# Kernel tuning notes

Measured on AMD Instinct MI355X. Metric: run time of the kernel, lower is better.

## Reference

```python
import jax, jax.numpy as jnp
import numpy as np
from jax import lax

B, T, LM, H = 16, 60, 63, 64   # batch, frames, landmark dim, lstm hidden
IMG_H, IMG_W = 240, 320
CONV_FEAT = 252                 # 4 * 7 * 9


def _conv(x, w, b, s):
    # x: [N, Cin, H, W], w: [Cout, Cin, kh, kw], VALID padding, stride s
    y = lax.conv_general_dilated(x, w, (s, s), 'VALID',
                                 dimension_numbers=('NCHW', 'OIHW', 'NCHW'))
    return y + b[None, :, None, None]


def setup_inputs() -> dict:
    key = jax.random.key(0)
    ks = jax.random.split(key, 24)
    s = 0.05
    d = {
        'input': jax.random.normal(ks[0], (B, T, LM), jnp.float32),
        'video': jax.random.uniform(ks[1], (B, T, IMG_H, IMG_W), jnp.float32),
        'W00': jax.random.normal(ks[2], (LM, LM), jnp.float32) * s,
        'b00': jnp.zeros((LM,), jnp.float32),
        'W01': jax.random.normal(ks[3], (64, LM), jnp.float32) * s,
        'b01': jnp.zeros((64,), jnp.float32),
        'Wc0': jax.random.normal(ks[4], (16, 1, 5, 5), jnp.float32) * s,
        'bc0': jnp.zeros((16,), jnp.float32),
        'Wc1': jax.random.normal(ks[5], (16, 16, 5, 5), jnp.float32) * s,
        'bc1': jnp.zeros((16,), jnp.float32),
        'Wc2': jax.random.normal(ks[6], (4, 16, 2, 2), jnp.float32) * s,
        'bc2': jnp.zeros((4,), jnp.float32),
        'Wih': jax.random.normal(ks[7], (4 * H, 64 + CONV_FEAT), jnp.float32) * s,
        'Whh': jax.random.normal(ks[8], (4 * H, H), jnp.float32) * s,
        'bih': jnp.zeros((4 * H,), jnp.float32),
        'bhh': jnp.zeros((4 * H,), jnp.float32),
        'W10': jax.random.normal(ks[9], (32, H), jnp.float32) * s,
        'b10': jnp.zeros((32,), jnp.float32),
        'W11': jax.random.normal(ks[10], (32, 32), jnp.float32) * s,
        'b11': jnp.zeros((32,), jnp.float32),
        'W12': jax.random.normal(ks[11], (256, 32), jnp.float32) * s,
        'b12': jnp.zeros((256,), jnp.float32),
    }
    return d


def reference(input, video, W00, b00, W01, b01, Wc0, bc0, Wc1, bc1, Wc2, bc2,
              Wih, Whh, bih, bhh, W10, b10, W11, b11, W12, b12):
    relu = jax.nn.relu
    # per-frame landmark MLP, vectorized over all frames: [B, T, 64]
    f = relu(jnp.einsum('btl,ml->btm', input, W00) + b00)
    f = relu(jnp.einsum('btl,ml->btm', f, W01) + b01)
    # per-frame conv features, all frames in one batched conv: [B*T, 1, 240, 320]
    v = video.reshape(B * T, 1, IMG_H, IMG_W)
    v = relu(_conv(v, Wc0, bc0, 4))          # [B*T, 16, 59, 79]
    v = relu(_conv(v, Wc1, bc1, 4))          # [B*T, 16, 14, 19]
    v = relu(_conv(v, Wc2, bc2, 2))          # [B*T, 4, 7, 9]
    v = v.reshape(B, T, CONV_FEAT)
    # frame inputs to LSTM: [B, T, 316]
    x = jnp.concatenate([f, v], axis=-1)
    # Torch semantics: LSTM called unbatched with 2D input [B, 316] per frame,
    # so the batch dim is consumed as a sequence; state carries across frames.
    # Total sequence is frame-major: [T, B, 316] -> [T*B, 316].
    seq = x.transpose(1, 0, 2).reshape(T * B, -1)

    def step(carry, xt):
        h, c = carry
        g = xt @ Wih.T + bih + h @ Whh.T + bhh
        i, fg, gg, o = jnp.split(g, 4)
        c = jax.nn.sigmoid(fg) * c + jax.nn.sigmoid(i) * jnp.tanh(gg)
        h = jax.nn.sigmoid(o) * jnp.tanh(c)
        return (h, c), h

    h0 = jnp.zeros((H,), seq.dtype)
    _, hs = lax.scan(step, (h0, h0), seq)    # [T*B, H]
    out = hs[-B:]                            # last frame's full output: [B, H]
    out = relu(out @ W10.T + b10)
    out = relu(out @ W11.T + b11)
    return out @ W12.T + b12                 # [B, 256]
```

## Files before the change

kernel.cpp:

```cpp
#include <hip/hip_runtime.h>
#include <math.h>

#define B_   16
#define T_   60
#define LMD  63
#define IH   240
#define IW   320
#define XDIM 316
#define NSEQ 960

#define X_BYTES   1213440
#define G_BYTES   983040

__device__ __forceinline__ float rl(float v, int k) {
    return __uint_as_float((unsigned)__builtin_amdgcn_readlane((int)__float_as_uint(v), k));
}
__device__ __forceinline__ float sig_f(float x) {
    return __builtin_amdgcn_rcpf(1.0f + __expf(-x));
}
__device__ __forceinline__ float tanh_f(float x) {
    return 1.0f - 2.0f * __builtin_amdgcn_rcpf(__expf(2.0f * x) + 1.0f);
}

__global__ void k_mlp(const float* __restrict__ inp,
                      const float* __restrict__ W00, const float* __restrict__ b00,
                      const float* __restrict__ W01, const float* __restrict__ b01,
                      float* __restrict__ X) {
    __shared__ float x0s[LMD], f1s[LMD];
    int bt = blockIdx.x;
    int b = bt / T_, t = bt % T_;
    int s = t * B_ + b;
    int m = threadIdx.x;
    if (m < LMD) x0s[m] = inp[bt * LMD + m];
    __syncthreads();
    if (m < LMD) {
        const float* wr = W00 + m * LMD;
        float a0 = 0.f, a1 = 0.f, a2 = 0.f, a3 = 0.f;
        for (int k = 0; k < 60; k += 4) {
            a0 += x0s[k + 0] * wr[k + 0];
            a1 += x0s[k + 1] * wr[k + 1];
            a2 += x0s[k + 2] * wr[k + 2];
            a3 += x0s[k + 3] * wr[k + 3];
        }
        a0 += x0s[60] * wr[60]; a1 += x0s[61] * wr[61]; a2 += x0s[62] * wr[62];
        f1s[m] = fmaxf(((a0 + a1) + (a2 + a3)) + b00[m], 0.f);
    }
    __syncthreads();
    {
        const float* wr = W01 + m * LMD;
        float a0 = 0.f, a1 = 0.f, a2 = 0.f, a3 = 0.f;
        for (int k = 0; k < 60; k += 4) {
            a0 += f1s[k + 0] * wr[k + 0];
            a1 += f1s[k + 1] * wr[k + 1];
            a2 += f1s[k + 2] * wr[k + 2];
            a3 += f1s[k + 3] * wr[k + 3];
        }
        a0 += f1s[60] * wr[60]; a1 += f1s[61] * wr[61]; a2 += f1s[62] * wr[62];
        X[(size_t)s * XDIM + m] = fmaxf(((a0 + a1) + (a2 + a3)) + b01[m], 0.f);
    }
}

__global__ __launch_bounds__(256, 1) void k_conv(const float* __restrict__ video,
        const float* __restrict__ Wc0, const float* __restrict__ bc0,
        const float* __restrict__ Wc1, const float* __restrict__ bc1,
        const float* __restrict__ Wc2, const float* __restrict__ bc2,
        float* __restrict__ X) {
    __shared__ float W0T[26 * 16];
    __shared__ float band[16 * 408];
    __shared__ float part[19 * 4 * 17];
    __shared__ float c1L[14 * 19 * 17];
    int tid = threadIdx.x;
    int bt = blockIdx.x;
    int b = bt / T_, t = bt % T_;
    int s = t * B_ + b;
    const float* vid = video + (size_t)bt * (IH * IW);

    int ch1 = tid & 15, ic = tid >> 4;
    int wave = tid >> 6, lane = tid & 63;

    int d0 = tid / 79, c0c0 = tid % 79;
    int pos1 = tid + 256;
    bool has1 = (pos1 < 395);
    int d1 = has1 ? pos1 / 79 : 0, c0c1 = has1 ? pos1 % 79 : 0;

    for (int i = tid; i < 400; i += 256) { int ch = i / 25, tap = i % 25; W0T[tap * 16 + ch] = Wc0[i]; }
    if (tid < 16) W0T[25 * 16 + tid] = bc0[tid];
    float w1r[25];
#pragma unroll
    for (int tap = 0; tap < 25; ++tap)
        w1r[tap] = Wc1[(ch1 * 16 + ic) * 25 + tap];

    float PX0[25], PX1[25];
    {
        const float* vb = vid + (4 * d0) * IW + c0c0 * 4;
#pragma unroll
        for (int kr = 0; kr < 5; ++kr) {
            float4 v = *(const float4*)(vb + kr * IW);
            PX0[kr*5+0]=v.x; PX0[kr*5+1]=v.y; PX0[kr*5+2]=v.z; PX0[kr*5+3]=v.w;
            PX0[kr*5+4]=vb[kr*IW+4];
        }
        if (has1) {
            const float* vc = vid + (4 * d1) * IW + c0c1 * 4;
#pragma unroll
            for (int kr = 0; kr < 5; ++kr) {
                float4 v = *(const float4*)(vc + kr * IW);
                PX1[kr*5+0]=v.x; PX1[kr*5+1]=v.y; PX1[kr*5+2]=v.z; PX1[kr*5+3]=v.w;
                PX1[kr*5+4]=vc[kr*IW+4];
            }
        }
    }
    __syncthreads();

    for (int r1 = 0; r1 < 14; ++r1) {
        {
            float acc[16];
            {
                const float4* b4 = (const float4*)&W0T[25 * 16];
                float4 ba = b4[0], bb = b4[1], bc = b4[2], bd = b4[3];
                acc[0]=ba.x; acc[1]=ba.y; acc[2]=ba.z; acc[3]=ba.w;
                acc[4]=bb.x; acc[5]=bb.y; acc[6]=bb.z; acc[7]=bb.w;
                acc[8]=bc.x; acc[9]=bc.y; acc[10]=bc.z; acc[11]=bc.w;
                acc[12]=bd.x; acc[13]=bd.y; acc[14]=bd.z; acc[15]=bd.w;
            }
#pragma unroll
            for (int tap = 0; tap < 25; ++tap) {
                float p = PX0[tap];
                const float4* w4 = (const float4*)&W0T[tap * 16];
                float4 wa = w4[0], wb = w4[1], wc = w4[2], wd = w4[3];
                acc[0]+=p*wa.x; acc[1]+=p*wa.y; acc[2]+=p*wa.z; acc[3]+=p*wa.w;
                acc[4]+=p*wb.x; acc[5]+=p*wb.y; acc[6]+=p*wb.z; acc[7]+=p*wb.w;
                acc[8]+=p*wc.x; acc[9]+=p*wc.y; acc[10]+=p*wc.z; acc[11]+=p*wc.w;
                acc[12]+=p*wd.x; acc[13]+=p*wd.y; acc[14]+=p*wd.z; acc[15]+=p*wd.w;
            }
#pragma unroll
            for (int ch = 0; ch < 16; ++ch)
                band[ch * 408 + d0 * 80 + c0c0] = fmaxf(acc[ch], 0.f);
        }
        if (has1) {
            float acc[16];
            {
                const float4* b4 = (const float4*)&W0T[25 * 16];
                float4 ba = b4[0], bb = b4[1], bc = b4[2], bd = b4[3];
                acc[0]=ba.x; acc[1]=ba.y; acc[2]=ba.z; acc[3]=ba.w;
                acc[4]=bb.x; acc[5]=bb.y; acc[6]=bb.z; acc[7]=bb.w;
                acc[8]=bc.x; acc[9]=bc.y; acc[10]=bc.z; acc[11]=bc.w;
                acc[12]=bd.x; acc[13]=bd.y; acc[14]=bd.z; acc[15]=bd.w;
            }
#pragma unroll
            for (int tap = 0; tap < 25; ++tap) {
                float p = PX1[tap];
                const float4* w4 = (const float4*)&W0T[tap * 16];
                float4 wa = w4[0], wb = w4[1], wc = w4[2], wd = w4[3];
                acc[0]+=p*wa.x; acc[1]+=p*wa.y; acc[2]+=p*wa.z; acc[3]+=p*wa.w;
                acc[4]+=p*wb.x; acc[5]+=p*wb.y; acc[6]+=p*wb.z; acc[7]+=p*wb.w;
                acc[8]+=p*wc.x; acc[9]+=p*wc.y; acc[10]+=p*wc.z; acc[11]+=p*wc.w;
                acc[12]+=p*wd.x; acc[13]+=p*wd.y; acc[14]+=p*wd.z; acc[15]+=p*wd.w;
            }
#pragma unroll
            for (int ch = 0; ch < 16; ++ch)
                band[ch * 408 + d1 * 80 + c0c1] = fmaxf(acc[ch], 0.f);
        }

        if (r1 + 1 < 14) {
            const float* vb = vid + (16 * (r1+1) + 4 * d0) * IW + c0c0 * 4;
#pragma unroll
            for (int kr = 0; kr < 5; ++kr) {
                float4 v = *(const float4*)(vb + kr * IW);
                PX0[kr*5+0]=v.x; PX0[kr*5+1]=v.y; PX0[kr*5+2]=v.z; PX0[kr*5+3]=v.w;
                PX0[kr*5+4]=vb[kr*IW+4];
            }
            if (has1) {
                const float* vc = vid + (16 * (r1+1) + 4 * d1) * IW + c0c1 * 4;
#pragma unroll
                for (int kr = 0; kr < 5; ++kr) {
                    float4 v = *(const float4*)(vc + kr * IW);
                    PX1[kr*5+0]=v.x; PX1[kr*5+1]=v.y; PX1[kr*5+2]=v.z; PX1[kr*5+3]=v.w;
                    PX1[kr*5+4]=vc[kr*IW+4];
                }
            }
        }
        __syncthreads();

        const float* bb0 = &band[ic * 408];
        for (int c1c = 0; c1c < 19; ++c1c) {
            const float* bb = bb0 + c1c * 4;
            float a0, a1, a2, a3, a4;
            {
                float4 v = *(const float4*)(bb);       float sc = bb[4];
                a0 = v.x*w1r[0]  + v.y*w1r[1]  + v.z*w1r[2]  + v.w*w1r[3]  + sc*w1r[4];
            }
            {
                float4 v = *(const float4*)(bb + 80);  float sc = bb[84];
                a1 = v.x*w1r[5]  + v.y*w1r[6]  + v.z*w1r[7]  + v.w*w1r[8]  + sc*w1r[9];
            }
            {
                float4 v = *(const float4*)(bb + 160); float sc = bb[164];
                a2 = v.x*w1r[10] + v.y*w1r[11] + v.z*w1r[12] + v.w*w1r[13] + sc*w1r[14];
            }
            {
                float4 v = *(const float4*)(bb + 240); float sc = bb[244];
                a3 = v.x*w1r[15] + v.y*w1r[16] + v.z*w1r[17] + v.w*w1r[18] + sc*w1r[19];
            }
            {
                float4 v = *(const float4*)(bb + 320); float sc = bb[324];
                a4 = v.x*w1r[20] + v.y*w1r[21] + v.z*w1r[22] + v.w*w1r[23] + sc*w1r[24];
            }
            float p = ((a0 + a1) + (a2 + a3)) + a4;
            p += __shfl_xor(p, 16);
            p += __shfl_xor(p, 32);
            if (lane < 16)
                part[c1c * 68 + wave * 17 + ch1] = p;
        }
        __syncthreads();

        for (int o = tid; o < 304; o += 256) {
            int c1c = o >> 4, ch = o & 15;
            const float* pp = &part[c1c * 68 + ch];
            float v = bc1[ch] + pp[0] + pp[17] + pp[34] + pp[51];
            c1L[(r1 * 19 + c1c) * 17 + ch] = fmaxf(v, 0.f);
        }
        __syncthreads();
    }

    for (int o = tid; o < 252; o += 256) {
        int ch2 = o / 63, rr = (o / 9) % 7, cc = o % 9;
        float a = bc2[ch2];
        for (int ic2 = 0; ic2 < 16; ++ic2)
            for (int kr = 0; kr < 2; ++kr)
                for (int kc = 0; kc < 2; ++kc)
                    a += c1L[((2 * rr + kr) * 19 + 2 * cc + kc) * 17 + ic2] *
                         Wc2[((ch2 * 16 + ic2) * 2 + kr) * 2 + kc];
        X[(size_t)s * XDIM + 64 + o] = fmaxf(a, 0.f);
    }
}

__global__ void k_gpre(const float* __restrict__ X, const float* __restrict__ Wih,
                       const float* __restrict__ bih, const float* __restrict__ bhh,
                       float* __restrict__ G) {
    int s = blockIdx.x;
    int j = threadIdx.x;
    const float4* x4 = (const float4*)(X + (size_t)s * XDIM);
    const float4* w4 = (const float4*)(Wih + (size_t)j * XDIM);
    float a0 = 0.f, a1 = 0.f, a2 = 0.f, a3 = 0.f;
    for (int ko = 0; ko < 79; ++ko) {
        float4 w = w4[ko], x = x4[ko];
        a0 += w.x * x.x;
        a1 += w.y * x.y;
        a2 += w.z * x.z;
        a3 += w.w * x.w;
    }
    G[(size_t)s * 256 + j] = ((a0 + a1) + (a2 + a3)) + (bih[j] + bhh[j]);
}

#define REPW(M) M(0) M(1) M(2) M(3) M(4) M(5) M(6) M(7) \
                M(8) M(9) M(10) M(11) M(12) M(13) M(14) M(15)

__global__ __launch_bounds__(256)
__attribute__((amdgpu_waves_per_eu(1, 1)))
void k_scan(const float* __restrict__ G,
        const float* __restrict__ Whh,
        const float* __restrict__ W10, const float* __restrict__ b10,
        const float* __restrict__ W11, const float* __restrict__ b11,
        const float* __restrict__ W12, const float* __restrict__ b12,
        float* __restrict__ out) {
    __shared__ float act[2][256];
    __shared__ float hsL[16 * 64];
    __shared__ float m1s[32], m2s[32];
    int j = threadIdx.x;
    int w = j >> 6, l = j & 63;

#define DECLW(n) float4 wv##n;
    REPW(DECLW)
#undef DECLW
    {
        const float4* Wr = (const float4*)(Whh + (size_t)j * 64);
#define LOADW(n) wv##n = Wr[n];
        REPW(LOADW)
#undef LOADW
    }

    float h = 0.f, c = 0.f;
    float gcur = G[j];

#define STEPBODY(GNEXT_EXPR)                                              \
    {                                                                     \
        float gnext = (GNEXT_EXPR);                                       \
        float a0 = gcur, a1 = 0.f, a2 = 0.f, a3 = 0.f;                    \
        REPW(GFMA)                                                        \
        float g = (a0 + a1) + (a2 + a3);                                  \
        float av = (w == 2) ? tanh_f(g) : sig_f(g);                       \
        act[t & 1][j] = av;                                               \
        asm volatile("s_waitcnt lgkmcnt(0)\n\ts_barrier" ::: "memory");   \
        const float* ab = act[t & 1];                                     \
        float ai = ab[l], af = ab[64 + l], ag = ab[128 + l], ao = ab[192 + l]; \
        c = af * c + ai * ag;                                             \
        h = ao * tanh_f(c);                                               \
        gcur = gnext;                                                     \
    }
#define GFMA(n) {                                                         \
        float h0 = rl(h, 4*(n)+0), h1 = rl(h, 4*(n)+1);                   \
        float h2 = rl(h, 4*(n)+2), h3 = rl(h, 4*(n)+3);                   \
        a0 += h0 * wv##n.x; a1 += h1 * wv##n.y;                           \
        a2 += h2 * wv##n.z; a3 += h3 * wv##n.w;                           \
    }

    for (int t = 0; t < NSEQ - 16; ++t) {
        STEPBODY(G[(size_t)(t + 1) * 256 + j])
    }
    for (int t = NSEQ - 16; t < NSEQ; ++t) {
        STEPBODY((t + 1 < NSEQ) ? G[(size_t)(t + 1) * 256 + j] : 0.f)
        if (w == 0) hsL[(t - (NSEQ - 16)) * 64 + l] = h;
    }
#undef GFMA
#undef STEPBODY
    __syncthreads();

    for (int r = 0; r < 16; ++r) {
        if (j < 32) {
            float a = b10[j];
            for (int k = 0; k < 64; ++k) a += hsL[r * 64 + k] * W10[j * 64 + k];
            m1s[j] = fmaxf(a, 0.f);
        }
        __syncthreads();
        if (j < 32) {
            float a = b11[j];
            for (int k = 0; k < 32; ++k) a += m1s[k] * W11[j * 32 + k];
            m2s[j] = fmaxf(a, 0.f);
        }
        __syncthreads();
        {
            float a = b12[j];
            for (int k = 0; k < 32; ++k) a += m2s[k] * W12[j * 32 + k];
            out[r * 256 + j] = a;
        }
        __syncthreads();
    }
}

extern "C" void kernel_launch(void* const* d_in, const int* in_sizes, int n_in,
                              void* d_out, int out_size, void* d_ws, size_t ws_size,
                              hipStream_t stream) {
    const float* inp   = (const float*)d_in[0];
    const float* video = (const float*)d_in[1];
    const float* W00   = (const float*)d_in[2];
    const float* b00   = (const float*)d_in[3];
    const float* W01   = (const float*)d_in[4];
    const float* b01   = (const float*)d_in[5];
    const float* Wc0   = (const float*)d_in[6];
    const float* bc0   = (const float*)d_in[7];
    const float* Wc1   = (const float*)d_in[8];
    const float* bc1   = (const float*)d_in[9];
    const float* Wc2   = (const float*)d_in[10];
    const float* bc2   = (const float*)d_in[11];
    const float* Wih   = (const float*)d_in[12];
    const float* Whh   = (const float*)d_in[13];
    const float* bih   = (const float*)d_in[14];
    const float* bhh   = (const float*)d_in[15];
    const float* W10   = (const float*)d_in[16];
    const float* b10   = (const float*)d_in[17];
    const float* W11   = (const float*)d_in[18];
    const float* b11   = (const float*)d_in[19];
    const float* W12   = (const float*)d_in[20];
    const float* b12   = (const float*)d_in[21];

    float* X = (float*)d_ws;
    float* G = (float*)((char*)d_ws + X_BYTES);

    k_mlp <<<NSEQ, 64, 0, stream>>>(inp, W00, b00, W01, b01, X);
    k_conv<<<NSEQ, 256, 0, stream>>>(video, Wc0, bc0, Wc1, bc1, Wc2, bc2, X);
    k_gpre<<<NSEQ, 256, 0, stream>>>(X, Wih, bih, bhh, G);
    k_scan<<<1, 256, 0, stream>>>(G, Whh, W10, b10, W11, b11, W12, b12, (float*)d_out);
}
```

Baseline: 715.8 us.

## Fuse landmark MLP, conv stack and input-gate projection into one kernel

Merges the per-frame MLP, the conv feature extractor and the Wih input projection into a single kernel per sequence position, keeping the 316-wide feature row in shared memory instead of writing X to global memory and reading it back. This drops two kernel launches and the X round trip. Launch bounds are raised from 1 to 3 blocks per CU, which may constrain registers for the conv stage. Block indexing is changed to be frame-major.

```diff
diff --git a/kernel.cpp b/kernel.cpp
--- a/kernel.cpp
+++ b/kernel.cpp
@@ -9,7 +9,6 @@
 #define XDIM 316
 #define NSEQ 960
 
-#define X_BYTES   1213440
 #define G_BYTES   983040
 
 __device__ __forceinline__ float rl(float v, int k) {
@@ -22,19 +21,46 @@
     return 1.0f - 2.0f * __builtin_amdgcn_rcpf(__expf(2.0f * x) + 1.0f);
 }
 
-__global__ void k_mlp(const float* __restrict__ inp,
-                      const float* __restrict__ W00, const float* __restrict__ b00,
-                      const float* __restrict__ W01, const float* __restrict__ b01,
-                      float* __restrict__ X) {
-    __shared__ float x0s[LMD], f1s[LMD];
-    int bt = blockIdx.x;
-    int b = bt / T_, t = bt % T_;
-    int s = t * B_ + b;
-    int m = threadIdx.x;
-    if (m < LMD) x0s[m] = inp[bt * LMD + m];
-    __syncthreads();
-    if (m < LMD) {
-        const float* wr = W00 + m * LMD;
+__global__ __launch_bounds__(256, 3) void k_prod(
+        const float* __restrict__ inp,  const float* __restrict__ video,
+        const float* __restrict__ W00,  const float* __restrict__ b00,
+        const float* __restrict__ W01,  const float* __restrict__ b01,
+        const float* __restrict__ Wc0,  const float* __restrict__ bc0,
+        const float* __restrict__ Wc1,  const float* __restrict__ bc1,
+        const float* __restrict__ Wc2,  const float* __restrict__ bc2,
+        const float* __restrict__ Wih,  const float* __restrict__ bih,
+        const float* __restrict__ bhh,  float* __restrict__ G)
+{
+    __shared__ float W0T[26 * 16];
+    __shared__ float band[16 * 408];
+    __shared__ float part[19 * 4 * 17];
+    __shared__ float c1L[14 * 19 * 17];
+    __shared__ __align__(16) float xrow[XDIM];
+    __shared__ float x0s[64], f1s[64];
+    int tid = threadIdx.x;
+    int s = blockIdx.x;
+    int t = s >> 4, b = s & 15;
+    int bt = b * T_ + t;
+    const float* vid = video + (size_t)bt * (IH * IW);
+
+    int ch1 = tid & 15, ic = tid >> 4;
+    int wave = tid >> 6, lane = tid & 63;
+    int d0 = tid / 79, c0c0 = tid % 79;
+    int pos1 = tid + 256;
+    bool has1 = (pos1 < 395);
+    int d1 = has1 ? pos1 / 79 : 0, c0c1 = has1 ? pos1 % 79 : 0;
+
+    for (int i = tid; i < 400; i += 256) { int ch = i / 25, tap = i % 25; W0T[tap * 16 + ch] = Wc0[i]; }
+    if (tid < 16) W0T[25 * 16 + tid] = bc0[tid];
+    float w1r[25];
+#pragma unroll
+    for (int tap = 0; tap < 25; ++tap)
+        w1r[tap] = Wc1[(ch1 * 16 + ic) * 25 + tap];
+
+    if (tid < LMD) x0s[tid] = inp[bt * LMD + tid];
+    __syncthreads();
+    if (tid < LMD) {
+        const float* wr = W00 + tid * LMD;
         float a0 = 0.f, a1 = 0.f, a2 = 0.f, a3 = 0.f;
         for (int k = 0; k < 60; k += 4) {
             a0 += x0s[k + 0] * wr[k + 0];
@@ -43,11 +69,11 @@
             a3 += x0s[k + 3] * wr[k + 3];
         }
         a0 += x0s[60] * wr[60]; a1 += x0s[61] * wr[61]; a2 += x0s[62] * wr[62];
-        f1s[m] = fmaxf(((a0 + a1) + (a2 + a3)) + b00[m], 0.f);
-    }
-    __syncthreads();
-    {
-        const float* wr = W01 + m * LMD;
+        f1s[tid] = fmaxf(((a0 + a1) + (a2 + a3)) + b00[tid], 0.f);
+    }
+    __syncthreads();
+    if (tid < 64) {
+        const float* wr = W01 + tid * LMD;
         float a0 = 0.f, a1 = 0.f, a2 = 0.f, a3 = 0.f;
         for (int k = 0; k < 60; k += 4) {
             a0 += f1s[k + 0] * wr[k + 0];
@@ -56,39 +82,8 @@
             a3 += f1s[k + 3] * wr[k + 3];
         }
         a0 += f1s[60] * wr[60]; a1 += f1s[61] * wr[61]; a2 += f1s[62] * wr[62];
-        X[(size_t)s * XDIM + m] = fmaxf(((a0 + a1) + (a2 + a3)) + b01[m], 0.f);
-    }
-}
-
-__global__ __launch_bounds__(256, 1) void k_conv(const float* __restrict__ video,
-        const float* __restrict__ Wc0, const float* __restrict__ bc0,
-        const float* __restrict__ Wc1, const float* __restrict__ bc1,
-        const float* __restrict__ Wc2, const float* __restrict__ bc2,
-        float* __restrict__ X) {
-    __shared__ float W0T[26 * 16];
-    __shared__ float band[16 * 408];
-    __shared__ float part[19 * 4 * 17];
-    __shared__ float c1L[14 * 19 * 17];
-    int tid = threadIdx.x;
-    int bt = blockIdx.x;
-    int b = bt / T_, t = bt % T_;
-    int s = t * B_ + b;
-    const float* vid = video + (size_t)bt * (IH * IW);
-
-    int ch1 = tid & 15, ic = tid >> 4;
-    int wave = tid >> 6, lane = tid & 63;
-
-    int d0 = tid / 79, c0c0 = tid % 79;
-    int pos1 = tid + 256;
-    bool has1 = (pos1 < 395);
-    int d1 = has1 ? pos1 / 79 : 0, c0c1 = has1 ? pos1 % 79 : 0;
-
-    for (int i = tid; i < 400; i += 256) { int ch = i / 25, tap = i % 25; W0T[tap * 16 + ch] = Wc0[i]; }
-    if (tid < 16) W0T[25 * 16 + tid] = bc0[tid];
-    float w1r[25];
-#pragma unroll
-    for (int tap = 0; tap < 25; ++tap)
-        w1r[tap] = Wc1[(ch1 * 16 + ic) * 25 + tap];
+        xrow[tid] = fmaxf(((a0 + a1) + (a2 + a3)) + b01[tid], 0.f);
+    }
 
     float PX0[25], PX1[25];
     {
@@ -230,26 +225,23 @@
                 for (int kc = 0; kc < 2; ++kc)
                     a += c1L[((2 * rr + kr) * 19 + 2 * cc + kc) * 17 + ic2] *
                          Wc2[((ch2 * 16 + ic2) * 2 + kr) * 2 + kc];
-        X[(size_t)s * XDIM + 64 + o] = fmaxf(a, 0.f);
-    }
-}
-
-__global__ void k_gpre(const float* __restrict__ X, const float* __restrict__ Wih,
-                       const float* __restrict__ bih, const float* __restrict__ bhh,
-                       float* __restrict__ G) {
-    int s = blockIdx.x;
-    int j = threadIdx.x;
-    const float4* x4 = (const float4*)(X + (size_t)s * XDIM);
-    const float4* w4 = (const float4*)(Wih + (size_t)j * XDIM);
-    float a0 = 0.f, a1 = 0.f, a2 = 0.f, a3 = 0.f;
-    for (int ko = 0; ko < 79; ++ko) {
-        float4 w = w4[ko], x = x4[ko];
-        a0 += w.x * x.x;
-        a1 += w.y * x.y;
-        a2 += w.z * x.z;
-        a3 += w.w * x.w;
-    }
-    G[(size_t)s * 256 + j] = ((a0 + a1) + (a2 + a3)) + (bih[j] + bhh[j]);
+        xrow[64 + o] = fmaxf(a, 0.f);
+    }
+    __syncthreads();
+
+    {
+        const float4* x4 = (const float4*)xrow;
+        const float4* w4 = (const float4*)(Wih + (size_t)tid * XDIM);
+        float a0 = 0.f, a1 = 0.f, a2 = 0.f, a3 = 0.f;
+        for (int ko = 0; ko < 79; ++ko) {
+            float4 w = w4[ko], x = x4[ko];
+            a0 += w.x * x.x;
+            a1 += w.y * x.y;
+            a2 += w.z * x.z;
+            a3 += w.w * x.w;
+        }
+        G[(size_t)s * 256 + tid] = ((a0 + a1) + (a2 + a3)) + (bih[tid] + bhh[tid]);
+    }
 }
 
 #define REPW(M) M(0) M(1) M(2) M(3) M(4) M(5) M(6) M(7) \
@@ -363,11 +355,10 @@
     const float* W12   = (const float*)d_in[20];
     const float* b12   = (const float*)d_in[21];
 
-    float* X = (float*)d_ws;
-    float* G = (float*)((char*)d_ws + X_BYTES);
-
-    k_mlp <<<NSEQ, 64, 0, stream>>>(inp, W00, b00, W01, b01, X);
-    k_conv<<<NSEQ, 256, 0, stream>>>(video, Wc0, bc0, Wc1, bc1, Wc2, bc2, X);
-    k_gpre<<<NSEQ, 256, 0, stream>>>(X, Wih, bih, bhh, G);
+    float* G = (float*)d_ws;
+
+    k_prod<<<NSEQ, 256, 0, stream>>>(inp, video, W00, b00, W01, b01,
+                                     Wc0, bc0, Wc1, bc1, Wc2, bc2,
+                                     Wih, bih, bhh, G);
     k_scan<<<1, 256, 0, stream>>>(G, Whh, W10, b10, W11, b11, W12, b12, (float*)d_out);
 }
```

Measured after the change: 724.6 us. No clear change (+1.2%).

## Keep conv0 weights in registers and split output channels across thread quads

Applied to the files above, without the earlier changes.

The first conv stage drops the shared-memory transposed weight table. Each thread now holds 4 output channels' 25-tap weights in registers, and groups of 4 threads split the 16 channels for one output position, looping over 7 positions per band. Launch bounds are raised to allow 3 blocks per CU. The register prefetch of the next band's pixels is removed, so global loads now sit directly in the compute loop, and each pixel is loaded by 4 threads instead of 1. The aim is to cut LDS weight reads and raise occupancy, at the cost of more global load traffic and possible register spills under the tighter bound.

```diff
diff --git a/kernel.cpp b/kernel.cpp
--- a/kernel.cpp
+++ b/kernel.cpp
@@ -60,12 +60,11 @@
     }
 }
 
-__global__ __launch_bounds__(256, 1) void k_conv(const float* __restrict__ video,
+__global__ __launch_bounds__(256, 3) void k_conv(const float* __restrict__ video,
         const float* __restrict__ Wc0, const float* __restrict__ bc0,
         const float* __restrict__ Wc1, const float* __restrict__ bc1,
         const float* __restrict__ Wc2, const float* __restrict__ bc2,
         float* __restrict__ X) {
-    __shared__ float W0T[26 * 16];
     __shared__ float band[16 * 408];
     __shared__ float part[19 * 4 * 17];
     __shared__ float c1L[14 * 19 * 17];
@@ -78,105 +77,57 @@
     int ch1 = tid & 15, ic = tid >> 4;
     int wave = tid >> 6, lane = tid & 63;
 
-    int d0 = tid / 79, c0c0 = tid % 79;
-    int pos1 = tid + 256;
-    bool has1 = (pos1 < 395);
-    int d1 = has1 ? pos1 / 79 : 0, c0c1 = has1 ? pos1 % 79 : 0;
-
-    for (int i = tid; i < 400; i += 256) { int ch = i / 25, tap = i % 25; W0T[tap * 16 + ch] = Wc0[i]; }
-    if (tid < 16) W0T[25 * 16 + tid] = bc0[tid];
+    int q = tid & 3, pgrp = tid >> 2;
+
+    float w0a[25], w0b[25], w0c[25], w0d[25];
+#pragma unroll
+    for (int tap = 0; tap < 25; ++tap) {
+        w0a[tap] = Wc0[(4 * q + 0) * 25 + tap];
+        w0b[tap] = Wc0[(4 * q + 1) * 25 + tap];
+        w0c[tap] = Wc0[(4 * q + 2) * 25 + tap];
+        w0d[tap] = Wc0[(4 * q + 3) * 25 + tap];
+    }
+    float b0a = bc0[4 * q + 0], b0b = bc0[4 * q + 1];
+    float b0c = bc0[4 * q + 2], b0d = bc0[4 * q + 3];
+
     float w1r[25];
 #pragma unroll
     for (int tap = 0; tap < 25; ++tap)
         w1r[tap] = Wc1[(ch1 * 16 + ic) * 25 + tap];
 
-    float PX0[25], PX1[25];
-    {
-        const float* vb = vid + (4 * d0) * IW + c0c0 * 4;
-#pragma unroll
-        for (int kr = 0; kr < 5; ++kr) {
-            float4 v = *(const float4*)(vb + kr * IW);
-            PX0[kr*5+0]=v.x; PX0[kr*5+1]=v.y; PX0[kr*5+2]=v.z; PX0[kr*5+3]=v.w;
-            PX0[kr*5+4]=vb[kr*IW+4];
-        }
-        if (has1) {
-            const float* vc = vid + (4 * d1) * IW + c0c1 * 4;
-#pragma unroll
-            for (int kr = 0; kr < 5; ++kr) {
-                float4 v = *(const float4*)(vc + kr * IW);
-                PX1[kr*5+0]=v.x; PX1[kr*5+1]=v.y; PX1[kr*5+2]=v.z; PX1[kr*5+3]=v.w;
-                PX1[kr*5+4]=vc[kr*IW+4];
-            }
-        }
-    }
-    __syncthreads();
-
     for (int r1 = 0; r1 < 14; ++r1) {
         {
-            float acc[16];
-            {
-                const float4* b4 = (const float4*)&W0T[25 * 16];
-                float4 ba = b4[0], bb = b4[1], bc = b4[2], bd = b4[3];
-                acc[0]=ba.x; acc[1]=ba.y; acc[2]=ba.z; acc[3]=ba.w;
-                acc[4]=bb.x; acc[5]=bb.y; acc[6]=bb.z; acc[7]=bb.w;
-                acc[8]=bc.x; acc[9]=bc.y; acc[10]=bc.z; acc[11]=bc.w;
-                acc[12]=bd.x; acc[13]=bd.y; acc[14]=bd.z; acc[15]=bd.w;
-            }
+            int d = 0, c0c = pgrp;
 #pragma unroll
-            for (int tap = 0; tap < 25; ++tap) {
-                float p = PX0[tap];
-                const float4* w4 = (const float4*)&W0T[tap * 16];
-                float4 wa = w4[0], wb = w4[1], wc = w4[2], wd = w4[3];
-                acc[0]+=p*wa.x; acc[1]+=p*wa.y; acc[2]+=p*wa.z; acc[3]+=p*wa.w;
-                acc[4]+=p*wb.x; acc[5]+=p*wb.y; acc[6]+=p*wb.z; acc[7]+=p*wb.w;
-                acc[8]+=p*wc.x; acc[9]+=p*wc.y; acc[10]+=p*wc.z; acc[11]+=p*wc.w;
-                acc[12]+=p*wd.x; acc[13]+=p*wd.y; acc[14]+=p*wd.z; acc[15]+=p*wd.w;
-            }
+            for (int i = 0; i < 7; ++i) {
+                if (i < 6 || pgrp < 11) {
+                    const float* vb = vid + (16 * r1 + 4 * d) * IW + c0c * 4;
+                    float aa = b0a, ab = b0b, ac = b0c, ad = b0d;
 #pragma unroll
-            for (int ch = 0; ch < 16; ++ch)
-                band[ch * 408 + d0 * 80 + c0c0] = fmaxf(acc[ch], 0.f);
-        }
-        if (has1) {
-            float acc[16];
-            {
-                const float4* b4 = (const float4*)&W0T[25 * 16];
-                float4 ba = b4[0], bb = b4[1], bc = b4[2], bd = b4[3];
-                acc[0]=ba.x; acc[1]=ba.y; acc[2]=ba.z; acc[3]=ba.w;
-                acc[4]=bb.x; acc[5]=bb.y; acc[6]=bb.z; acc[7]=bb.w;
-                acc[8]=bc.x; acc[9]=bc.y; acc[10]=bc.z; acc[11]=bc.w;
-                acc[12]=bd.x; acc[13]=bd.y; acc[14]=bd.z; acc[15]=bd.w;
-            }
-#pragma unroll
-            for (int tap = 0; tap < 25; ++tap) {
-                float p = PX1[tap];
-                const float4* w4 = (const float4*)&W0T[tap * 16];
-                float4 wa = w4[0], wb = w4[1], wc = w4[2], wd = w4[3];
-                acc[0]+=p*wa.x; acc[1]+=p*wa.y; acc[2]+=p*wa.z; acc[3]+=p*wa.w;
-                acc[4]+=p*wb.x; acc[5]+=p*wb.y; acc[6]+=p*wb.z; acc[7]+=p*wb.w;
-                acc[8]+=p*wc.x; acc[9]+=p*wc.y; acc[10]+=p*wc.z; acc[11]+=p*wc.w;
-                acc[12]+=p*wd.x; acc[13]+=p*wd.y; acc[14]+=p*wd.z; acc[15]+=p*wd.w;
-            }
-#pragma unroll
-            for (int ch = 0; ch < 16; ++ch)
-                band[ch * 408 + d1 * 80 + c0c1] = fmaxf(acc[ch], 0.f);
-        }
-
-        if (r1 + 1 < 14) {
-            const float* vb = vid + (16 * (r1+1) + 4 * d0) * IW + c0c0 * 4;
-#pragma unroll
-            for (int kr = 0; kr < 5; ++kr) {
-                float4 v = *(const float4*)(vb + kr * IW);
-                PX0[kr*5+0]=v.x; PX0[kr*5+1]=v.y; PX0[kr*5+2]=v.z; PX0[kr*5+3]=v.w;
-                PX0[kr*5+4]=vb[kr*IW+4];
-            }
-            if (has1) {
-                const float* vc = vid + (16 * (r1+1) + 4 * d1) * IW + c0c1 * 4;
-#pragma unroll
-                for (int kr = 0; kr < 5; ++kr) {
-                    float4 v = *(const float4*)(vc + kr * IW);
-                    PX1[kr*5+0]=v.x; PX1[kr*5+1]=v.y; PX1[kr*5+2]=v.z; PX1[kr*5+3]=v.w;
-                    PX1[kr*5+4]=vc[kr*IW+4];
+                    for (int kr = 0; kr < 5; ++kr) {
+                        float4 v = *(const float4*)(vb + kr * IW);
+                        float p4 = vb[kr * IW + 4];
+                        aa += v.x * w0a[5*kr+0]; aa += v.y * w0a[5*kr+1];
+                        aa += v.z * w0a[5*kr+2]; aa += v.w * w0a[5*kr+3];
+                        aa += p4  * w0a[5*kr+4];
+                        ab += v.x * w0b[5*kr+0]; ab += v.y * w0b[5*kr+1];
+                        ab += v.z * w0b[5*kr+2]; ab += v.w * w0b[5*kr+3];
+                        ab += p4  * w0b[5*kr+4];
+                        ac += v.x * w0c[5*kr+0]; ac += v.y * w0c[5*kr+1];
+                        ac += v.z * w0c[5*kr+2]; ac += v.w * w0c[5*kr+3];
+                        ac += p4  * w0c[5*kr+4];
+                        ad += v.x * w0d[5*kr+0]; ad += v.y * w0d[5*kr+1];
+                        ad += v.z * w0d[5*kr+2]; ad += v.w * w0d[5*kr+3];
+                        ad += p4  * w0d[5*kr+4];
+                    }
+                    int bo = d * 80 + c0c;
+                    band[(4 * q + 0) * 408 + bo] = fmaxf(aa, 0.f);
+                    band[(4 * q + 1) * 408 + bo] = fmaxf(ab, 0.f);
+                    band[(4 * q + 2) * 408 + bo] = fmaxf(ac, 0.f);
+                    band[(4 * q + 3) * 408 + bo] = fmaxf(ad, 0.f);
                 }
+                c0c += 64;
+                if (c0c >= 79) { c0c -= 79; ++d; }
             }
         }
         __syncthreads();
```

Result: slower. 1.155 ms (+61.3%).
